# Optimization experiments

Hardware: AMD Instinct MI355X
Metric: run time of the kernel (lower is better)

Reference implementation:

```python
import jax, jax.numpy as jnp
import numpy as np

N_S, N_H, N_ACT, N_LINKS = 512, 256, 7, 9
AXIS_LIST = jnp.array([2, 0, 2, 2, 2, 0, 2])
LINK_LIST = jnp.arange(N_ACT)
ROT_SIGN = jnp.array([1., 1., 1., 1., -1., 1., 1.], dtype=jnp.float32)  # rot[..., 4] *= -1
MASS = jnp.array([105.98, 105.98, 314.98, 279.2, 105.98, 105.98, 243.66], dtype=jnp.float32)
TOTAL_MASS = jnp.sum(MASS) + 100000.0 + 243.66
DIAGS = jnp.array([[12.19, 12.19, 3.061], [12.19, 12.19, 3.061], [15.41, 2094.71, 2103.19],
                   [9.522, 1966.28, 1966.28], [8.305, 3.061, 8.0386], [12.13, 12.13, 3.061],
                   [9.336, 44.41, 44.41]], dtype=jnp.float32)
INERTIAL = DIAGS[:, :, None] * jnp.eye(3, dtype=jnp.float32)          # (7,3,3) diagonal inertias
SUM_MASS = jnp.cumsum(MASS[::-1])[::-1].reshape(1, 1, 1, N_ACT)       # suffix sums
SUM_INERTIAL = jnp.cumsum(INERTIAL[::-1], axis=0)[::-1]               # (7,3,3)
TRIL = jnp.tril(jnp.ones((N_ACT, N_ACT), dtype=jnp.float32)).reshape(1, 1, N_ACT, 1, N_ACT)
MASS_MASK = MASS.reshape(1, 1, N_ACT, 1, 1) * TRIL                    # mass_H_wphi_mask
TF0 = jnp.array([[1, 0, 0, 0], [0, -1, 0, 0], [0, 0, 1.3, 6], [0, 0, 0, 1]], dtype=jnp.float32)
COM0 = jnp.array([[1, 0, 0, 0], [0, 1, 0, 0], [0, 0, 1, 0.5], [0, 0, 0, 1]], dtype=jnp.float32)
BASE_COM = (TF0 @ COM0)[:3, 3] * 243.66 / (100000.0 + 243.66)


def _skew(p):
    x, y, z = p[..., 0], p[..., 1], p[..., 2]
    z0 = jnp.zeros_like(x)
    return jnp.stack([jnp.stack([z0, -z, y], -1),
                      jnp.stack([z, z0, -x], -1),
                      jnp.stack([-y, x, z0], -1)], -2)


def _skew_mul(p):
    x, y, z = p[..., 0], p[..., 1], p[..., 2]
    r2 = x * x + y * y + z * z
    row0 = jnp.stack([r2 - x * x, -x * y, -x * z], -1)
    row1 = jnp.stack([-x * y, r2 - y * y, -y * z], -1)
    row2 = jnp.stack([-x * z, -y * z, r2 - z * z], -1)
    return jnp.stack([row0, row1, row2], -2)


def _inv3(H):
    a, b, c = H[..., 0, 0], H[..., 0, 1], H[..., 0, 2]
    d, e, f = H[..., 1, 0], H[..., 1, 1], H[..., 1, 2]
    g, h, i = H[..., 2, 0], H[..., 2, 1], H[..., 2, 2]
    det = a * (e * i - f * h) - b * (d * i - f * g) + c * (d * h - e * g)
    C11 = e * i - f * h; C12 = -(b * i - c * h); C13 = b * f - c * e
    C21 = -(d * i - f * g); C22 = a * i - c * g; C23 = -(a * f - c * d)
    C31 = d * h - e * g; C32 = -(a * h - b * g); C33 = a * e - b * d
    adj = jnp.stack([jnp.stack([C11, C21, C31], -1),
                     jnp.stack([C12, C22, C32], -1),
                     jnp.stack([C13, C23, C33], -1)], -2)
    return adj / det[..., None, None]


def _forward(com_list, link_pose_list, bm):
    rot = link_pose_list[:, :, :3, AXIS_LIST, LINK_LIST] * ROT_SIGN  # (n,h,3,7)
    if bm:
        del_p = com_list[:, :, :, :N_ACT] - link_pose_list[:, :, :3, 3, :N_ACT]  # (n,h,3,7)
        del_p_a = jnp.swapaxes(del_p, -1, -2)                                     # (n,h,7,3)
        del_p_skew = _skew(del_p_a)                                               # (n,h,7,3,3)
        jacob_t = jnp.cross(rot, del_p, axis=2)                                   # (n,h,3,7)
        jacob_tw = jacob_t * SUM_MASS
        H_w = jnp.sum(INERTIAL.reshape(1, 1, N_ACT, 3, 3)
                      + MASS.reshape(1, 1, N_ACT, 1, 1) * _skew_mul(del_p_a), axis=2)  # (n,h,3,3)
        term1 = jnp.einsum('aij,shja->shia', SUM_INERTIAL, rot)                   # (n,h,3,7)
        jac_w = jacob_t[:, :, None] * MASS_MASK                                   # (n,h,7,3,7)
        term2 = jnp.einsum('shaij,shajk->shik', del_p_skew, jac_w)                # (n,h,3,7)
        H_wphi = term1 + term2
        system_com = jnp.einsum('ntci,i->ntc', com_list, MASS) / TOTAL_MASS       # (n,h,3)
        r_og = _skew(system_com - BASE_COM)                                       # (n,h,3,3)
        H_s = TOTAL_MASS * (r_og @ r_og) + H_w
        H_theta = H_wphi - r_og @ jacob_tw
        H_inv = _inv3(H_s)
        top = -(jacob_tw / TOTAL_MASS + r_og @ (H_inv @ H_theta))
        bot = -(H_inv @ H_theta)
        return jnp.concatenate([top, bot], axis=2)                                # (n,h,6,7)
    else:
        del_p = link_pose_list[:, :, :3, 3, -2][..., None] - link_pose_list[:, :, :3, 3, :N_ACT]
        jt = jnp.cross(rot, del_p, axis=2)
        return jnp.concatenate([jt, rot], axis=2)


def setup_inputs() -> dict:
    key = jax.random.key(0)
    k1, k2 = jax.random.split(key)
    com_list = jax.random.normal(k1, (N_S, N_H, 3, N_ACT), dtype=jnp.float32)
    link_pose_list = jax.random.normal(k2, (N_S, N_H, 4, 4, N_LINKS), dtype=jnp.float32)
    return {"com_list": com_list, "link_pose_list": link_pose_list, "bm": 1}


def reference(com_list, link_pose_list, bm):
    return _forward(com_list, link_pose_list, bm)
```

## Files before the change

### kernel.cpp

```cpp
#include <hip/hip_runtime.h>


__global__ __launch_bounds__(256) void canadarm_jacob_kernel(
    const float* __restrict__ com,
    const float* __restrict__ pose,
    const int* __restrict__ bm_ptr,
    float* __restrict__ out,
    int n_items)
{
    const int idx = blockIdx.x * blockDim.x + threadIdx.x;
    if (idx >= n_items) return;

    const float MASS[7] = {105.98f, 105.98f, 314.98f, 279.2f, 105.98f, 105.98f, 243.66f};
    const float SUMM[7] = {1261.76f, 1155.78f, 1049.80f, 734.82f, 455.62f, 349.64f, 243.66f};
    const float SIX[7] = {79.083f, 66.893f, 54.703f, 39.293f, 29.771f, 21.466f, 9.336f};
    const float SIY[7] = {4144.971f, 4132.781f, 4120.591f, 2025.881f, 59.601f, 56.540f, 44.410f};
    const float SIZ[7] = {4131.1016f, 4128.0406f, 4124.9796f, 2021.7896f, 55.5096f, 47.471f, 44.410f};
    const float TM     = 101505.42f;
    const float INV_TM = 1.0f / 101505.42f;
    const float BCZ    = 6.65f * 243.66f / 100243.66f;

    const float4* Pb = reinterpret_cast<const float4*>(pose) + (size_t)idx * 36;
    float rot[3][7];
    float tr[3][8];
#pragma unroll
    for (int r = 0; r < 3; ++r) {
        const float4 q0 = Pb[r * 9 + 0];
        const float4 q1 = Pb[r * 9 + 1];
        const float4 q4 = Pb[r * 9 + 4];
        const float4 q5 = Pb[r * 9 + 5];
        const float4 q6 = Pb[r * 9 + 6];
        const float4 q7 = Pb[r * 9 + 7];
        const float4 q8 = Pb[r * 9 + 8];
        rot[r][0] = q4.z;
        rot[r][1] = q0.y;
        rot[r][2] = q5.x;
        rot[r][3] = q5.y;
        rot[r][4] = -q5.z;
        rot[r][5] = q1.y;
        rot[r][6] = q6.x;
        tr[r][0] = q6.w;
        tr[r][1] = q7.x; tr[r][2] = q7.y; tr[r][3] = q7.z; tr[r][4] = q7.w;
        tr[r][5] = q8.x; tr[r][6] = q8.y; tr[r][7] = q8.z;
    }

    const int bm = bm_ptr[0];
    float o[42];

    if (bm) {
        const float* C = com + (size_t)idx * 21;
        float cm[3][7];
#pragma unroll
        for (int r = 0; r < 3; ++r)
#pragma unroll
            for (int i = 0; i < 7; ++i) cm[r][i] = C[r * 7 + i];

        float scx = 0.f, scy = 0.f, scz = 0.f;
#pragma unroll
        for (int i = 0; i < 7; ++i) {
            scx += cm[0][i] * MASS[i];
            scy += cm[1][i] * MASS[i];
            scz += cm[2][i] * MASS[i];
        }
        const float vx = scx * INV_TM;
        const float vy = scy * INV_TM;
        const float vz = scz * INV_TM - BCZ;

        float dp[3][7], jt[3][7];
        float hxx = SIX[0], hyy = SIY[0], hzz = SIZ[0];
        float hxy = 0.f, hxz = 0.f, hyz = 0.f;
#pragma unroll
        for (int i = 0; i < 7; ++i) {
            const float x = cm[0][i] - tr[0][i];
            const float y = cm[1][i] - tr[1][i];
            const float z = cm[2][i] - tr[2][i];
            dp[0][i] = x; dp[1][i] = y; dp[2][i] = z;
            jt[0][i] = rot[1][i] * z - rot[2][i] * y;
            jt[1][i] = rot[2][i] * x - rot[0][i] * z;
            jt[2][i] = rot[0][i] * y - rot[1][i] * x;
            const float m = MASS[i];
            hxx += m * (y * y + z * z);
            hyy += m * (x * x + z * z);
            hzz += m * (x * x + y * y);
            hxy -= m * x * y;
            hxz -= m * x * z;
            hyz -= m * y * z;
        }

        float wx[7], wy[7], wz[7];
        wx[6] = MASS[6] * dp[0][6];
        wy[6] = MASS[6] * dp[1][6];
        wz[6] = MASS[6] * dp[2][6];
#pragma unroll
        for (int k = 5; k >= 0; --k) {
            wx[k] = wx[k + 1] + MASS[k] * dp[0][k];
            wy[k] = wy[k + 1] + MASS[k] * dp[1][k];
            wz[k] = wz[k + 1] + MASS[k] * dp[2][k];
        }

        const float vv = vx * vx + vy * vy + vz * vz;
        const float a  = hxx + TM * (vx * vx - vv);
        const float b  = hxy + TM * (vx * vy);
        const float c  = hxz + TM * (vx * vz);
        const float e  = hyy + TM * (vy * vy - vv);
        const float f  = hyz + TM * (vy * vz);
        const float i9 = hzz + TM * (vz * vz - vv);

        const float c11 = e * i9 - f * f;
        const float c12 = c * f - b * i9;
        const float c13 = b * f - e * c;
        const float det = a * c11 + b * c12 + c * c13;
        const float rdet = 1.0f / det;
        const float i00 = c11 * rdet;
        const float i01 = c12 * rdet;
        const float i02 = c13 * rdet;
        const float i11 = (a * i9 - c * c) * rdet;
        const float i12 = (c * b - a * f) * rdet;
        const float i22 = (a * e - b * b) * rdet;

#pragma unroll
        for (int k = 0; k < 7; ++k) {
            const float ux = wx[k] - SUMM[k] * vx;
            const float uy = wy[k] - SUMM[k] * vy;
            const float uz = wz[k] - SUMM[k] * vz;
            const float jx = jt[0][k], jy = jt[1][k], jz = jt[2][k];
            const float htx = SIX[k] * rot[0][k] + uy * jz - uz * jy;
            const float hty = SIY[k] * rot[1][k] + uz * jx - ux * jz;
            const float htz = SIZ[k] * rot[2][k] + ux * jy - uy * jx;
            const float bx = i00 * htx + i01 * hty + i02 * htz;
            const float by = i01 * htx + i11 * hty + i12 * htz;
            const float bz = i02 * htx + i12 * hty + i22 * htz;
            const float s = SUMM[k] * INV_TM;
            o[0 * 7 + k] = -(s * jx + vy * bz - vz * by);
            o[1 * 7 + k] = -(s * jy + vz * bx - vx * bz);
            o[2 * 7 + k] = -(s * jz + vx * by - vy * bx);
            o[3 * 7 + k] = -bx;
            o[4 * 7 + k] = -by;
            o[5 * 7 + k] = -bz;
        }
    } else {
#pragma unroll
        for (int k = 0; k < 7; ++k) {
            const float dx = tr[0][7] - tr[0][k];
            const float dy = tr[1][7] - tr[1][k];
            const float dz = tr[2][7] - tr[2][k];
            o[0 * 7 + k] = rot[1][k] * dz - rot[2][k] * dy;
            o[1 * 7 + k] = rot[2][k] * dx - rot[0][k] * dz;
            o[2 * 7 + k] = rot[0][k] * dy - rot[1][k] * dx;
            o[3 * 7 + k] = rot[0][k];
            o[4 * 7 + k] = rot[1][k];
            o[5 * 7 + k] = rot[2][k];
        }
    }

    float2* Ob = reinterpret_cast<float2*>(out + (size_t)idx * 42);
#pragma unroll
    for (int t = 0; t < 21; ++t) Ob[t] = make_float2(o[2 * t], o[2 * t + 1]);
}

extern "C" void kernel_launch(void* const* d_in, const int* in_sizes, int n_in,
                              void* d_out, int out_size, void* d_ws, size_t ws_size,
                              hipStream_t stream) {
    const float* com  = (const float*)d_in[0];
    const float* pose = (const float*)d_in[1];
    const int*   bm   = (const int*)d_in[2];
    float* out = (float*)d_out;

    const int n_items = in_sizes[0] / 21;
    const int block = 256;
    const int grid = (n_items + block - 1) / block;
    canadarm_jacob_kernel<<<grid, block, 0, stream>>>(com, pose, bm, out, n_items);
}
```

Baseline: 125.3 us.

## Stage com input and output through LDS for coalesced vector accesses

Loads each block's com slice cooperatively with float4 into shared memory, and writes results to LDS first so they can be stored with coalesced float4 writes. This replaces the strided per-thread 21-float reads and 42-float writes, which coalesce poorly. The pose loads stay strided per thread. In exchange it uses 43 KB of LDS per block, which limits occupancy, and adds block barriers. The bounds check is removed, so it assumes n_items is a multiple of the block size, and LDS reads at stride 21/42 may hit bank conflicts.

```diff
diff --git a/kernel.cpp b/kernel.cpp
--- a/kernel.cpp
+++ b/kernel.cpp
@@ -1,15 +1,19 @@
 #include <hip/hip_runtime.h>
 
 
-__global__ __launch_bounds__(256) void canadarm_jacob_kernel(
+#define BLK 256
+
+__global__ __launch_bounds__(BLK) void canadarm_jacob_kernel(
     const float* __restrict__ com,
     const float* __restrict__ pose,
     const int* __restrict__ bm_ptr,
     float* __restrict__ out,
     int n_items)
 {
-    const int idx = blockIdx.x * blockDim.x + threadIdx.x;
-    if (idx >= n_items) return;
+    __shared__ float lds[BLK * 42];
+
+    const int tid = threadIdx.x;
+    const int idx = blockIdx.x * BLK + tid;
 
     const float MASS[7] = {105.98f, 105.98f, 314.98f, 279.2f, 105.98f, 105.98f, 243.66f};
     const float SUMM[7] = {1261.76f, 1155.78f, 1049.80f, 734.82f, 455.62f, 349.64f, 243.66f};
@@ -19,6 +23,15 @@
     const float TM     = 101505.42f;
     const float INV_TM = 1.0f / 101505.42f;
     const float BCZ    = 6.65f * 243.66f / 100243.66f;
+
+    {
+        const float4* Cb4 = reinterpret_cast<const float4*>(com) + (size_t)blockIdx.x * (BLK * 21 / 4);
+        float4* L4 = reinterpret_cast<float4*>(lds);
+#pragma unroll
+        for (int i = 0; i < 5; ++i) L4[tid + i * BLK] = Cb4[tid + i * BLK];
+        if (tid < BLK * 21 / 4 - 5 * BLK) L4[tid + 5 * BLK] = Cb4[tid + 5 * BLK];
+    }
+    __syncthreads();
 
     const float4* Pb = reinterpret_cast<const float4*>(pose) + (size_t)idx * 36;
     float rot[3][7];
@@ -48,12 +61,11 @@
     float o[42];
 
     if (bm) {
-        const float* C = com + (size_t)idx * 21;
         float cm[3][7];
 #pragma unroll
         for (int r = 0; r < 3; ++r)
 #pragma unroll
-            for (int i = 0; i < 7; ++i) cm[r][i] = C[r * 7 + i];
+            for (int i = 0; i < 7; ++i) cm[r][i] = lds[tid * 21 + r * 7 + i];
 
         float scx = 0.f, scy = 0.f, scz = 0.f;
 #pragma unroll
@@ -153,9 +165,18 @@
         }
     }
 
-    float2* Ob = reinterpret_cast<float2*>(out + (size_t)idx * 42);
+    __syncthreads();
 #pragma unroll
-    for (int t = 0; t < 21; ++t) Ob[t] = make_float2(o[2 * t], o[2 * t + 1]);
+    for (int j = 0; j < 42; ++j) lds[tid * 42 + j] = o[j];
+    __syncthreads();
+
+    {
+        float4* Ob4 = reinterpret_cast<float4*>(out) + (size_t)blockIdx.x * (BLK * 42 / 4);
+        const float4* L4 = reinterpret_cast<const float4*>(lds);
+#pragma unroll
+        for (int i = 0; i < 10; ++i) Ob4[tid + i * BLK] = L4[tid + i * BLK];
+        if (tid < BLK * 42 / 4 - 10 * BLK) Ob4[tid + 10 * BLK] = L4[tid + 10 * BLK];
+    }
 }
 
 extern "C" void kernel_launch(void* const* d_in, const int* in_sizes, int n_in,
@@ -167,7 +188,6 @@
     float* out = (float*)d_out;
 
     const int n_items = in_sizes[0] / 21;
-    const int block = 256;
-    const int grid = (n_items + block - 1) / block;
-    canadarm_jacob_kernel<<<grid, block, 0, stream>>>(com, pose, bm, out, n_items);
+    const int grid = (n_items + BLK - 1) / BLK;
+    canadarm_jacob_kernel<<<grid, BLK, 0, stream>>>(com, pose, bm, out, n_items);
 }
```

Result: no change. 125.8 us (+0.4%).

## Stage pose and com loads into LDS via async global_load_lds double buffering

Applied to the files above, without the earlier changes.

Each 64-thread block now handles four tiles of 64 items. The needed pose float4s and the com data are staged into shared memory with direct global-to-LDS loads, and the next tile's loads are double-buffered so they overlap compute on the current one. This replaces strided per-thread global loads with coalesced lane-contiguous transfers and skips the unused pose columns. In exchange it uses one-wave blocks with manual waitcnt synchronisation and drops the bounds check, so it assumes the item count divides by 256.

```diff
diff --git a/kernel.cpp b/kernel.cpp
--- a/kernel.cpp
+++ b/kernel.cpp
@@ -1,15 +1,57 @@
 #include <hip/hip_runtime.h>
 
 
-__global__ __launch_bounds__(256) void canadarm_jacob_kernel(
+#define IPB 64
+#define NB  4
+#define NDMA 27
+
+typedef const __attribute__((address_space(1))) void GAS;
+typedef __attribute__((address_space(3))) void LAS;
+
+__global__ __launch_bounds__(64, 1) void canadarm_jacob_kernel(
     const float* __restrict__ com,
     const float* __restrict__ pose,
     const int* __restrict__ bm_ptr,
-    float* __restrict__ out,
-    int n_items)
+    float* __restrict__ out)
 {
-    const int idx = blockIdx.x * blockDim.x + threadIdx.x;
-    if (idx >= n_items) return;
+    __shared__ float4 poseL[2][IPB * 21];
+    __shared__ float4 comL[2][384];
+
+    const int lane = threadIdx.x;
+    const int base_item = blockIdx.x * (NB * IPB);
+
+    int psrc[21];
+#pragma unroll
+    for (int j = 0; j < 21; ++j) {
+        const int d  = j * 64 + lane;
+        const int it = d / 21;
+        const int li = d - it * 21;
+        const int r  = li / 7;
+        const int q  = li - r * 7;
+        psrc[j] = it * 36 + 9 * r + (q < 2 ? q : q + 2);
+    }
+    int csrc[6];
+#pragma unroll
+    for (int i = 0; i < 6; ++i) {
+        const int c = i * 64 + lane;
+        csrc[i] = c < 336 ? c : 335;
+    }
+
+    const float4* Pb = reinterpret_cast<const float4*>(pose);
+    const float4* Cb = reinterpret_cast<const float4*>(com);
+
+    auto ISSUE = [&](int t, int b) {
+        const float4* P0 = Pb + (size_t)(base_item + t * IPB) * 36;
+        const float4* C0 = Cb + (size_t)(base_item + t * IPB) * 21 / 4;
+#pragma unroll
+        for (int j = 0; j < 21; ++j)
+            __builtin_amdgcn_global_load_lds((GAS*)(P0 + psrc[j]),
+                                             (LAS*)(&poseL[b][j * 64]), 16, 0, 0);
+#pragma unroll
+        for (int i = 0; i < 6; ++i)
+            __builtin_amdgcn_global_load_lds((GAS*)(C0 + csrc[i]),
+                                             (LAS*)(&comL[b][i * 64]), 16, 0, 0);
+    };
 
     const float MASS[7] = {105.98f, 105.98f, 314.98f, 279.2f, 105.98f, 105.98f, 243.66f};
     const float SUMM[7] = {1261.76f, 1155.78f, 1049.80f, 734.82f, 455.62f, 349.64f, 243.66f};
@@ -20,142 +62,158 @@
     const float INV_TM = 1.0f / 101505.42f;
     const float BCZ    = 6.65f * 243.66f / 100243.66f;
 
-    const float4* Pb = reinterpret_cast<const float4*>(pose) + (size_t)idx * 36;
-    float rot[3][7];
-    float tr[3][8];
-#pragma unroll
-    for (int r = 0; r < 3; ++r) {
-        const float4 q0 = Pb[r * 9 + 0];
-        const float4 q1 = Pb[r * 9 + 1];
-        const float4 q4 = Pb[r * 9 + 4];
-        const float4 q5 = Pb[r * 9 + 5];
-        const float4 q6 = Pb[r * 9 + 6];
-        const float4 q7 = Pb[r * 9 + 7];
-        const float4 q8 = Pb[r * 9 + 8];
-        rot[r][0] = q4.z;
-        rot[r][1] = q0.y;
-        rot[r][2] = q5.x;
-        rot[r][3] = q5.y;
-        rot[r][4] = -q5.z;
-        rot[r][5] = q1.y;
-        rot[r][6] = q6.x;
-        tr[r][0] = q6.w;
-        tr[r][1] = q7.x; tr[r][2] = q7.y; tr[r][3] = q7.z; tr[r][4] = q7.w;
-        tr[r][5] = q8.x; tr[r][6] = q8.y; tr[r][7] = q8.z;
+    const int bm = bm_ptr[0];
+
+    ISSUE(0, 0);
+
+#pragma unroll
+    for (int t = 0; t < NB; ++t) {
+        const int b = t & 1;
+
+        asm volatile("s_waitcnt lgkmcnt(0)" ::: "memory");
+        if (t + 1 < NB) {
+            ISSUE(t + 1, b ^ 1);
+            asm volatile("s_waitcnt vmcnt(27)" ::: "memory");
+        } else {
+            asm volatile("s_waitcnt vmcnt(0)" ::: "memory");
+        }
+
+        const float4* L = &poseL[b][lane * 21];
+        float rot[3][7];
+        float tr[3][8];
+#pragma unroll
+        for (int r = 0; r < 3; ++r) {
+            const float4 q0 = L[7 * r + 0];
+            const float4 q1 = L[7 * r + 1];
+            const float4 q4 = L[7 * r + 2];
+            const float4 q5 = L[7 * r + 3];
+            const float4 q6 = L[7 * r + 4];
+            const float4 q7 = L[7 * r + 5];
+            const float4 q8 = L[7 * r + 6];
+            rot[r][0] = q4.z;
+            rot[r][1] = q0.y;
+            rot[r][2] = q5.x;
+            rot[r][3] = q5.y;
+            rot[r][4] = -q5.z;
+            rot[r][5] = q1.y;
+            rot[r][6] = q6.x;
+            tr[r][0] = q6.w;
+            tr[r][1] = q7.x; tr[r][2] = q7.y; tr[r][3] = q7.z; tr[r][4] = q7.w;
+            tr[r][5] = q8.x; tr[r][6] = q8.y; tr[r][7] = q8.z;
+        }
+
+        float o[42];
+
+        if (bm) {
+            const float* Cf = reinterpret_cast<const float*>(&comL[b][0]) + lane * 21;
+            float cm[3][7];
+#pragma unroll
+            for (int r = 0; r < 3; ++r)
+#pragma unroll
+                for (int i = 0; i < 7; ++i) cm[r][i] = Cf[r * 7 + i];
+
+            float scx = 0.f, scy = 0.f, scz = 0.f;
+#pragma unroll
+            for (int i = 0; i < 7; ++i) {
+                scx += cm[0][i] * MASS[i];
+                scy += cm[1][i] * MASS[i];
+                scz += cm[2][i] * MASS[i];
+            }
+            const float vx = scx * INV_TM;
+            const float vy = scy * INV_TM;
+            const float vz = scz * INV_TM - BCZ;
+
+            float dp[3][7], jt[3][7];
+            float hxx = SIX[0], hyy = SIY[0], hzz = SIZ[0];
+            float hxy = 0.f, hxz = 0.f, hyz = 0.f;
+#pragma unroll
+            for (int i = 0; i < 7; ++i) {
+                const float x = cm[0][i] - tr[0][i];
+                const float y = cm[1][i] - tr[1][i];
+                const float z = cm[2][i] - tr[2][i];
+                dp[0][i] = x; dp[1][i] = y; dp[2][i] = z;
+                jt[0][i] = rot[1][i] * z - rot[2][i] * y;
+                jt[1][i] = rot[2][i] * x - rot[0][i] * z;
+                jt[2][i] = rot[0][i] * y - rot[1][i] * x;
+                const float m = MASS[i];
+                hxx += m * (y * y + z * z);
+                hyy += m * (x * x + z * z);
+                hzz += m * (x * x + y * y);
+                hxy -= m * x * y;
+                hxz -= m * x * z;
+                hyz -= m * y * z;
+            }
+
+            float wx[7], wy[7], wz[7];
+            wx[6] = MASS[6] * dp[0][6];
+            wy[6] = MASS[6] * dp[1][6];
+            wz[6] = MASS[6] * dp[2][6];
+#pragma unroll
+            for (int k = 5; k >= 0; --k) {
+                wx[k] = wx[k + 1] + MASS[k] * dp[0][k];
+                wy[k] = wy[k + 1] + MASS[k] * dp[1][k];
+                wz[k] = wz[k + 1] + MASS[k] * dp[2][k];
+            }
+
+            const float vv = vx * vx + vy * vy + vz * vz;
+            const float a  = hxx + TM * (vx * vx - vv);
+            const float bb = hxy + TM * (vx * vy);
+            const float cc = hxz + TM * (vx * vz);
+            const float e  = hyy + TM * (vy * vy - vv);
+            const float f  = hyz + TM * (vy * vz);
+            const float i9 = hzz + TM * (vz * vz - vv);
+
+            const float c11 = e * i9 - f * f;
+            const float c12 = cc * f - bb * i9;
+            const float c13 = bb * f - e * cc;
+            const float det = a * c11 + bb * c12 + cc * c13;
+            const float rdet = 1.0f / det;
+            const float i00 = c11 * rdet;
+            const float i01 = c12 * rdet;
+            const float i02 = c13 * rdet;
+            const float i11 = (a * i9 - cc * cc) * rdet;
+            const float i12 = (cc * bb - a * f) * rdet;
+            const float i22 = (a * e - bb * bb) * rdet;
+
+#pragma unroll
+            for (int k = 0; k < 7; ++k) {
+                const float ux = wx[k] - SUMM[k] * vx;
+                const float uy = wy[k] - SUMM[k] * vy;
+                const float uz = wz[k] - SUMM[k] * vz;
+                const float jx = jt[0][k], jy = jt[1][k], jz = jt[2][k];
+                const float htx = SIX[k] * rot[0][k] + uy * jz - uz * jy;
+                const float hty = SIY[k] * rot[1][k] + uz * jx - ux * jz;
+                const float htz = SIZ[k] * rot[2][k] + ux * jy - uy * jx;
+                const float bx = i00 * htx + i01 * hty + i02 * htz;
+                const float by = i01 * htx + i11 * hty + i12 * htz;
+                const float bz = i02 * htx + i12 * hty + i22 * htz;
+                const float s = SUMM[k] * INV_TM;
+                o[0 * 7 + k] = -(s * jx + vy * bz - vz * by);
+                o[1 * 7 + k] = -(s * jy + vz * bx - vx * bz);
+                o[2 * 7 + k] = -(s * jz + vx * by - vy * bx);
+                o[3 * 7 + k] = -bx;
+                o[4 * 7 + k] = -by;
+                o[5 * 7 + k] = -bz;
+            }
+        } else {
+#pragma unroll
+            for (int k = 0; k < 7; ++k) {
+                const float dx = tr[0][7] - tr[0][k];
+                const float dy = tr[1][7] - tr[1][k];
+                const float dz = tr[2][7] - tr[2][k];
+                o[0 * 7 + k] = rot[1][k] * dz - rot[2][k] * dy;
+                o[1 * 7 + k] = rot[2][k] * dx - rot[0][k] * dz;
+                o[2 * 7 + k] = rot[0][k] * dy - rot[1][k] * dx;
+                o[3 * 7 + k] = rot[0][k];
+                o[4 * 7 + k] = rot[1][k];
+                o[5 * 7 + k] = rot[2][k];
+            }
+        }
+
+        float2* Ob = reinterpret_cast<float2*>(out + (size_t)(base_item + t * IPB + lane) * 42);
+#pragma unroll
+        for (int j = 0; j < 21; ++j) Ob[j] = make_float2(o[2 * j], o[2 * j + 1]);
     }
-
-    const int bm = bm_ptr[0];
-    float o[42];
-
-    if (bm) {
-        const float* C = com + (size_t)idx * 21;
-        float cm[3][7];
-#pragma unroll
-        for (int r = 0; r < 3; ++r)
-#pragma unroll
-            for (int i = 0; i < 7; ++i) cm[r][i] = C[r * 7 + i];
-
-        float scx = 0.f, scy = 0.f, scz = 0.f;
-#pragma unroll
-        for (int i = 0; i < 7; ++i) {
-            scx += cm[0][i] * MASS[i];
-            scy += cm[1][i] * MASS[i];
-            scz += cm[2][i] * MASS[i];
-        }
-        const float vx = scx * INV_TM;
-        const float vy = scy * INV_TM;
-        const float vz = scz * INV_TM - BCZ;
-
-        float dp[3][7], jt[3][7];
-        float hxx = SIX[0], hyy = SIY[0], hzz = SIZ[0];
-        float hxy = 0.f, hxz = 0.f, hyz = 0.f;
-#pragma unroll
-        for (int i = 0; i < 7; ++i) {
-            const float x = cm[0][i] - tr[0][i];
-            const float y = cm[1][i] - tr[1][i];
-            const float z = cm[2][i] - tr[2][i];
-            dp[0][i] = x; dp[1][i] = y; dp[2][i] = z;
-            jt[0][i] = rot[1][i] * z - rot[2][i] * y;
-            jt[1][i] = rot[2][i] * x - rot[0][i] * z;
-            jt[2][i] = rot[0][i] * y - rot[1][i] * x;
-            const float m = MASS[i];
-            hxx += m * (y * y + z * z);
-            hyy += m * (x * x + z * z);
-            hzz += m * (x * x + y * y);
-            hxy -= m * x * y;
-            hxz -= m * x * z;
-            hyz -= m * y * z;
-        }
-
-        float wx[7], wy[7], wz[7];
-        wx[6] = MASS[6] * dp[0][6];
-        wy[6] = MASS[6] * dp[1][6];
-        wz[6] = MASS[6] * dp[2][6];
-#pragma unroll
-        for (int k = 5; k >= 0; --k) {
-            wx[k] = wx[k + 1] + MASS[k] * dp[0][k];
-            wy[k] = wy[k + 1] + MASS[k] * dp[1][k];
-            wz[k] = wz[k + 1] + MASS[k] * dp[2][k];
-        }
-
-        const float vv = vx * vx + vy * vy + vz * vz;
-        const float a  = hxx + TM * (vx * vx - vv);
-        const float b  = hxy + TM * (vx * vy);
-        const float c  = hxz + TM * (vx * vz);
-        const float e  = hyy + TM * (vy * vy - vv);
-        const float f  = hyz + TM * (vy * vz);
-        const float i9 = hzz + TM * (vz * vz - vv);
-
-        const float c11 = e * i9 - f * f;
-        const float c12 = c * f - b * i9;
-        const float c13 = b * f - e * c;
-        const float det = a * c11 + b * c12 + c * c13;
-        const float rdet = 1.0f / det;
-        const float i00 = c11 * rdet;
-        const float i01 = c12 * rdet;
-        const float i02 = c13 * rdet;
-        const float i11 = (a * i9 - c * c) * rdet;
-        const float i12 = (c * b - a * f) * rdet;
-        const float i22 = (a * e - b * b) * rdet;
-
-#pragma unroll
-        for (int k = 0; k < 7; ++k) {
-            const float ux = wx[k] - SUMM[k] * vx;
-            const float uy = wy[k] - SUMM[k] * vy;
-            const float uz = wz[k] - SUMM[k] * vz;
-            const float jx = jt[0][k], jy = jt[1][k], jz = jt[2][k];
-            const float htx = SIX[k] * rot[0][k] + uy * jz - uz * jy;
-            const float hty = SIY[k] * rot[1][k] + uz * jx - ux * jz;
-            const float htz = SIZ[k] * rot[2][k] + ux * jy - uy * jx;
-            const float bx = i00 * htx + i01 * hty + i02 * htz;
-            const float by = i01 * htx + i11 * hty + i12 * htz;
-            const float bz = i02 * htx + i12 * hty + i22 * htz;
-            const float s = SUMM[k] * INV_TM;
-            o[0 * 7 + k] = -(s * jx + vy * bz - vz * by);
-            o[1 * 7 + k] = -(s * jy + vz * bx - vx * bz);
-            o[2 * 7 + k] = -(s * jz + vx * by - vy * bx);
-            o[3 * 7 + k] = -bx;
-            o[4 * 7 + k] = -by;
-            o[5 * 7 + k] = -bz;
-        }
-    } else {
-#pragma unroll
-        for (int k = 0; k < 7; ++k) {
-            const float dx = tr[0][7] - tr[0][k];
-            const float dy = tr[1][7] - tr[1][k];
-            const float dz = tr[2][7] - tr[2][k];
-            o[0 * 7 + k] = rot[1][k] * dz - rot[2][k] * dy;
-            o[1 * 7 + k] = rot[2][k] * dx - rot[0][k] * dz;
-            o[2 * 7 + k] = rot[0][k] * dy - rot[1][k] * dx;
-            o[3 * 7 + k] = rot[0][k];
-            o[4 * 7 + k] = rot[1][k];
-            o[5 * 7 + k] = rot[2][k];
-        }
-    }
-
-    float2* Ob = reinterpret_cast<float2*>(out + (size_t)idx * 42);
-#pragma unroll
-    for (int t = 0; t < 21; ++t) Ob[t] = make_float2(o[2 * t], o[2 * t + 1]);
 }
 
 extern "C" void kernel_launch(void* const* d_in, const int* in_sizes, int n_in,
@@ -167,7 +225,6 @@
     float* out = (float*)d_out;
 
     const int n_items = in_sizes[0] / 21;
-    const int block = 256;
-    const int grid = (n_items + block - 1) / block;
-    canadarm_jacob_kernel<<<grid, block, 0, stream>>>(com, pose, bm, out, n_items);
+    const int grid = n_items / (NB * IPB);
+    canadarm_jacob_kernel<<<grid, 64, 0, stream>>>(com, pose, bm, out);
 }
```

After: 128.0 us. 2.2% more time.
